# Kernel optimization log

Hardware: AMD Instinct MI355X
Metric: run time of the kernel (lower is better)

The kernel has to match this reference:

```python
import jax, jax.numpy as jnp
import numpy as np

N_LAYERS = 6
D_MODEL = 512
D_FFN = 2048
N_STATE = 64
KSIZE = 31
BATCH = 8
SEQ = 2048
IN_SIZE = 80


def _ln(x, g, b, eps=1e-5):
    m = jnp.mean(x, axis=-1, keepdims=True)
    v = jnp.mean((x - m) ** 2, axis=-1, keepdims=True)
    return (x - m) * jax.lax.rsqrt(v + eps) * g + b


def _ffn(x, g, b, w1, b1, w2, b2):
    # LayerNorm -> Linear(D->F) -> GELU -> Linear(F->D)  (PositionalwiseFeedForward)
    h = jax.nn.gelu(_ln(x, g, b) @ w1 + b1)
    return h @ w2 + b2


def _dss(x, lam_re, lam_im, c_re, c_im, d_skip, log_dt, w_out, b_out):
    # Diagonal state-space (DSS-EXP): generate length-T kernel from diagonal poles,
    # apply causal conv via FFT, skip D*u, GELU, GLU output projection.
    Bx, T, H = x.shape
    dt = jnp.exp(log_dt)
    lam = -jnp.exp(lam_re) + 1j * lam_im                        # [N] stable poles (Re<0)
    P = jnp.exp(lam[:, None] * (dt * jnp.arange(T))[None, :])   # [N, T]
    C = c_re + 1j * c_im                                        # [H, N]
    kern = jnp.einsum('hn,nt->ht', C, P).real * dt              # [H, T]
    u = x.transpose(0, 2, 1)                                    # [B, H, T]
    n = 2 * T
    y = jnp.fft.irfft(jnp.fft.rfft(u, n=n) * jnp.fft.rfft(kern, n=n), n=n)[..., :T]
    y = y + d_skip[None, :, None] * u
    y = jax.nn.gelu(y.transpose(0, 2, 1))                       # [B, T, H]
    z = y @ w_out + b_out                                       # [B, T, 2H]
    a, g = jnp.split(z, 2, axis=-1)
    return a * jax.nn.sigmoid(g)                                # GLU


def _conv_module(x, g1, b1, bw, bb, dw, db, g2, b2, lw, lb):
    # LN -> 1x1 conv to 2D + GLU -> depthwise conv (SAME, k=31) -> LN -> GELU -> Linear
    y = _ln(x, g1, b1)
    y = y @ bw.T + bb                                           # [B, T, 2D]
    a, g = jnp.split(y, 2, axis=-1)
    y = a * jax.nn.sigmoid(g)                                   # GLU over channels
    yc = y.transpose(0, 2, 1)                                   # [B, D, T]
    yc = jax.lax.conv_general_dilated(
        yc, dw[:, None, :], (1,), 'SAME',
        feature_group_count=yc.shape[1],
        dimension_numbers=('NCH', 'OIH', 'NCH'))
    yc = yc + db[None, :, None]
    y = jax.nn.gelu(_ln(yc.transpose(0, 2, 1), g2, b2))
    return y @ lw.T + lb


def _forward(src, speaker_embs, src_w, src_b,
             ffn1_ln_g, ffn1_ln_b, ffn1_w1, ffn1_b1, ffn1_w2, ffn1_b2,
             norm1_g, norm1_b,
             lam_re, lam_im, c_re, c_im, ssm_d, log_dt, dss_out_w, dss_out_b,
             conv_ln_g, conv_ln_b, bneck_w, bneck_b, dw_w, dw_b,
             conv_ln2_g, conv_ln2_b, conv_lin_w, conv_lin_b,
             ffn2_ln_g, ffn2_ln_b, ffn2_w1, ffn2_b1, ffn2_w2, ffn2_b2,
             norm2_g, norm2_b, final_g, final_b):
    x = src @ src_w + src_b                                     # custom_src_module Linear
    for i in range(N_LAYERS):
        x = x + 0.5 * _ffn(x, ffn1_ln_g[i], ffn1_ln_b[i], ffn1_w1[i], ffn1_b1[i], ffn1_w2[i], ffn1_b2[i])
        skip = x
        x = _ln(x, norm1_g[i], norm1_b[i])
        x = _dss(x, lam_re[i], lam_im[i], c_re[i], c_im[i], ssm_d[i], log_dt[i], dss_out_w[i], dss_out_b[i])
        x = x + skip
        x = x + _conv_module(x, conv_ln_g[i], conv_ln_b[i], bneck_w[i], bneck_b[i], dw_w[i], dw_b[i],
                             conv_ln2_g[i], conv_ln2_b[i], conv_lin_w[i], conv_lin_b[i])
        x = _ln(x + 0.5 * _ffn(x, ffn2_ln_g[i], ffn2_ln_b[i], ffn2_w1[i], ffn2_b1[i], ffn2_w2[i], ffn2_b2[i]),
                norm2_g[i], norm2_b[i])
    x = _ln(x, final_g, final_b, eps=1e-6)
    return x + speaker_embs


def setup_inputs() -> dict:
    key = jax.random.key(0)
    ks = iter(jax.random.split(key, 64))
    def rn(shape, s=0.02):
        return (jax.random.normal(next(ks), shape) * s).astype(jnp.float32)
    L, D, F, N, K = N_LAYERS, D_MODEL, D_FFN, N_STATE, KSIZE
    return dict(
        src=jax.random.normal(next(ks), (BATCH, SEQ, IN_SIZE), dtype=jnp.float32),
        speaker_embs=jax.random.normal(next(ks), (BATCH, 1, D), dtype=jnp.float32),
        src_w=rn((IN_SIZE, D)), src_b=jnp.zeros((D,), jnp.float32),
        ffn1_ln_g=jnp.ones((L, D), jnp.float32), ffn1_ln_b=jnp.zeros((L, D), jnp.float32),
        ffn1_w1=rn((L, D, F)), ffn1_b1=jnp.zeros((L, F), jnp.float32),
        ffn1_w2=rn((L, F, D)), ffn1_b2=jnp.zeros((L, D), jnp.float32),
        norm1_g=jnp.ones((L, D), jnp.float32), norm1_b=jnp.zeros((L, D), jnp.float32),
        lam_re=rn((L, N), 0.5), lam_im=rn((L, N), 3.0),
        c_re=rn((L, D, N), 0.1), c_im=rn((L, D, N), 0.1),
        ssm_d=rn((L, D), 1.0), log_dt=jnp.full((L,), float(np.log(0.01)), jnp.float32),
        dss_out_w=rn((L, D, 2 * D)), dss_out_b=jnp.zeros((L, 2 * D), jnp.float32),
        conv_ln_g=jnp.ones((L, D), jnp.float32), conv_ln_b=jnp.zeros((L, D), jnp.float32),
        bneck_w=rn((L, 2 * D, D)), bneck_b=jnp.zeros((L, 2 * D), jnp.float32),
        dw_w=rn((L, D, K), 0.1), dw_b=jnp.zeros((L, D), jnp.float32),
        conv_ln2_g=jnp.ones((L, D), jnp.float32), conv_ln2_b=jnp.zeros((L, D), jnp.float32),
        conv_lin_w=rn((L, D, D)), conv_lin_b=jnp.zeros((L, D), jnp.float32),
        ffn2_ln_g=jnp.ones((L, D), jnp.float32), ffn2_ln_b=jnp.zeros((L, D), jnp.float32),
        ffn2_w1=rn((L, D, F)), ffn2_b1=jnp.zeros((L, F), jnp.float32),
        ffn2_w2=rn((L, F, D)), ffn2_b2=jnp.zeros((L, D), jnp.float32),
        norm2_g=jnp.ones((L, D), jnp.float32), norm2_b=jnp.zeros((L, D), jnp.float32),
        final_g=jnp.ones((D,), jnp.float32), final_b=jnp.zeros((D,), jnp.float32),
    )


def reference(src, speaker_embs, src_w, src_b,
              ffn1_ln_g, ffn1_ln_b, ffn1_w1, ffn1_b1, ffn1_w2, ffn1_b2,
              norm1_g, norm1_b,
              lam_re, lam_im, c_re, c_im, ssm_d, log_dt, dss_out_w, dss_out_b,
              conv_ln_g, conv_ln_b, bneck_w, bneck_b, dw_w, dw_b,
              conv_ln2_g, conv_ln2_b, conv_lin_w, conv_lin_b,
              ffn2_ln_g, ffn2_ln_b, ffn2_w1, ffn2_b1, ffn2_w2, ffn2_b2,
              norm2_g, norm2_b, final_g, final_b):
    return _forward(src, speaker_embs, src_w, src_b,
                    ffn1_ln_g, ffn1_ln_b, ffn1_w1, ffn1_b1, ffn1_w2, ffn1_b2,
                    norm1_g, norm1_b,
                    lam_re, lam_im, c_re, c_im, ssm_d, log_dt, dss_out_w, dss_out_b,
                    conv_ln_g, conv_ln_b, bneck_w, bneck_b, dw_w, dw_b,
                    conv_ln2_g, conv_ln2_b, conv_lin_w, conv_lin_b,
                    ffn2_ln_g, ffn2_ln_b, ffn2_w1, ffn2_b1, ffn2_w2, ffn2_b2,
                    norm2_g, norm2_b, final_g, final_b)
```

## Files before the change

### kernel.cpp

```cpp
#include <hip/hip_runtime.h>
#include <hip/hip_bf16.h>
#include <stdint.h>


#define NL 6
#define TT 2048
#define BB 8
#define DD 512
#define FF 2048
#define ROWS (BB*TT)

typedef __attribute__((ext_vector_type(4))) float f32x4;
typedef __attribute__((ext_vector_type(8))) short s16x8;

#define DEVI __device__ __forceinline__

DEVI float bf2f(uint32_t u) { union { uint32_t i; float f; } v; v.i = u << 16; return v.f; }
DEVI uint16_t f2bf(float f) {
    union { float f; uint32_t i; } v; v.f = f;
    uint32_t x = v.i;
    return (uint16_t)((x + 0x7fffu + ((x >> 16) & 1u)) >> 16);
}
DEVI float gelu_f(float x) {
    float x3 = x * x * x;
    float a  = 0.7978845608028654f * (x + 0.044715f * x3);
    float e  = __expf(2.0f * a);
    float t  = 1.0f - 2.0f / (e + 1.0f);
    return 0.5f * x * (1.0f + t);
}
DEVI float sigm(float x) { return 1.0f / (1.0f + __expf(-x)); }

DEVI void gload16(const uint16_t* g, uint16_t* l) {
    __builtin_amdgcn_global_load_lds((const __attribute__((address_space(1))) void*)g,
                                     (__attribute__((address_space(3))) void*)l, 16, 0, 0);
}

__global__ void k_wtrans(const float* __restrict__ src, uint16_t* __restrict__ dst,
                         int K, int N) {
    __shared__ float tile[32][33];
    int l = blockIdx.z;
    const float* s = src + (size_t)l * K * N;
    uint16_t*    d = dst + (size_t)l * N * K;
    int n0 = blockIdx.x * 32, k0 = blockIdx.y * 32;
    int tx = threadIdx.x, ty = threadIdx.y;
#pragma unroll
    for (int i = 0; i < 4; i++) {
        int k = k0 + ty + i * 8;
        tile[ty + i * 8][tx] = s[(size_t)k * N + n0 + tx];
    }
    __syncthreads();
#pragma unroll
    for (int i = 0; i < 4; i++) {
        int n = n0 + ty + i * 8;
        d[(size_t)n * K + k0 + tx] = f2bf(tile[tx][ty + i * 8]);
    }
}
__global__ void k_wcvt(const float* __restrict__ src, uint16_t* __restrict__ dst, int n) {
    int i = blockIdx.x * 256 + threadIdx.x;
    if (i < n) dst[i] = f2bf(src[i]);
}
__global__ void k_dwt(const float* __restrict__ dw, float* __restrict__ dwt) {
    int i = blockIdx.x * 256 + threadIdx.x;
    int tot = NL * DD * 31;
    if (i >= tot) return;
    int l = i / (DD * 31), r = i % (DD * 31), d = r / 31, k = r % 31;
    dwt[(size_t)l * 31 * DD + k * DD + d] = dw[i];
}
__global__ void k_srcpad(const float* __restrict__ src, uint16_t* __restrict__ dst) {
    int i = blockIdx.x * 256 + threadIdx.x;
    if (i >= ROWS * 96) return;
    int r = i / 96, c = i - r * 96;
    dst[i] = (c < 80) ? f2bf(src[(size_t)r * 80 + c]) : (uint16_t)0;
}
__global__ void k_wsrcpad(const float* __restrict__ w, uint16_t* __restrict__ dst) {
    int i = blockIdx.x * 256 + threadIdx.x;
    if (i >= DD * 96) return;
    int n = i / 96, k = i - n * 96;
    dst[i] = (k < 80) ? f2bf(w[(size_t)k * DD + n]) : (uint16_t)0;
}

template <int MODE>
__global__ void k_ln(const float* __restrict__ in, void* __restrict__ outp,
                     const float* __restrict__ gam, const float* __restrict__ bet,
                     const float* __restrict__ spk, float eps) {
    int row  = blockIdx.x * 4 + (threadIdx.x >> 6);
    int lane = threadIdx.x & 63;
    const float* x = in + (size_t)row * DD;
    float4 a0 = *(const float4*)&x[lane * 4];
    float4 a1 = *(const float4*)&x[256 + lane * 4];
    float v[8] = {a0.x, a0.y, a0.z, a0.w, a1.x, a1.y, a1.z, a1.w};
    float s = 0.f, q = 0.f;
#pragma unroll
    for (int i = 0; i < 8; i++) { s += v[i]; q += v[i] * v[i]; }
#pragma unroll
    for (int m = 1; m < 64; m <<= 1) { s += __shfl_xor(s, m); q += __shfl_xor(q, m); }
    float mean = s * (1.0f / 512.0f);
    float var  = fmaxf(q * (1.0f / 512.0f) - mean * mean, 0.0f);
    float inv  = rsqrtf(var + eps);
    float4 g0 = *(const float4*)&gam[lane * 4];
    float4 g1 = *(const float4*)&gam[256 + lane * 4];
    float4 b0 = *(const float4*)&bet[lane * 4];
    float4 b1 = *(const float4*)&bet[256 + lane * 4];
    float gv[8] = {g0.x, g0.y, g0.z, g0.w, g1.x, g1.y, g1.z, g1.w};
    float bv[8] = {b0.x, b0.y, b0.z, b0.w, b1.x, b1.y, b1.z, b1.w};
    float y[8];
#pragma unroll
    for (int i = 0; i < 8; i++) y[i] = (v[i] - mean) * inv * gv[i] + bv[i];
    if (MODE == 1) {
#pragma unroll
        for (int i = 0; i < 8; i++) y[i] = gelu_f(y[i]);
    }
    if (MODE == 0 || MODE == 1) {
        uint16_t* o = (uint16_t*)outp + (size_t)row * DD;
        uint2 p0, p1;
        p0.x = (uint32_t)f2bf(y[0]) | ((uint32_t)f2bf(y[1]) << 16);
        p0.y = (uint32_t)f2bf(y[2]) | ((uint32_t)f2bf(y[3]) << 16);
        p1.x = (uint32_t)f2bf(y[4]) | ((uint32_t)f2bf(y[5]) << 16);
        p1.y = (uint32_t)f2bf(y[6]) | ((uint32_t)f2bf(y[7]) << 16);
        *(uint2*)&o[lane * 4]       = p0;
        *(uint2*)&o[256 + lane * 4] = p1;
    } else {
        float* o = (float*)outp + (size_t)row * DD;
        if (MODE == 3) {
            const float* sp = spk + (size_t)(row >> 11) * DD;
            float4 s0 = *(const float4*)&sp[lane * 4];
            float4 s1 = *(const float4*)&sp[256 + lane * 4];
            y[0] += s0.x; y[1] += s0.y; y[2] += s0.z; y[3] += s0.w;
            y[4] += s1.x; y[5] += s1.y; y[6] += s1.z; y[7] += s1.w;
        }
        *(float4*)&o[lane * 4]       = make_float4(y[0], y[1], y[2], y[3]);
        *(float4*)&o[256 + lane * 4] = make_float4(y[4], y[5], y[6], y[7]);
    }
}

template <int MODE>
__global__ __launch_bounds__(256) void k_gemm(
    const uint16_t* __restrict__ A, const uint16_t* __restrict__ Bt,
    const float* __restrict__ bias, int M, int N, int K,
    void* __restrict__ outp, float* __restrict__ X) {
    __shared__ __align__(16) uint16_t As[128 * 32];
    __shared__ __align__(16) uint16_t Bs[128 * 32];
    int tid = threadIdx.x;
    int m0 = blockIdx.x * 128, n0 = blockIdx.y * 128;
    int wave = tid >> 6, lane = tid & 63;
    int wm = (wave >> 1) * 64, wn = (wave & 1) * 64;
    int l15 = lane & 15, l16 = lane >> 4;

    const uint16_t* gA = A  + (size_t)(m0 + 32 * wave + l15) * K + l16 * 8;
    const uint16_t* gB = Bt + (size_t)(n0 + 32 * wave + l15) * K + l16 * 8;
    uint16_t* lA0 = &As[(2 * wave) * 512];
    uint16_t* lA1 = &As[(2 * wave + 1) * 512];
    uint16_t* lB0 = &Bs[(2 * wave) * 512];
    uint16_t* lB1 = &Bs[(2 * wave + 1) * 512];
    size_t rowskip = (size_t)16 * K;

    f32x4 acc[4][4];
#pragma unroll
    for (int i = 0; i < 4; i++)
#pragma unroll
        for (int j = 0; j < 4; j++) acc[i][j] = (f32x4){0.f, 0.f, 0.f, 0.f};

    for (int kt = 0; kt < K; kt += 32) {
        gload16(gA + kt, lA0);
        gload16(gA + rowskip + kt, lA1);
        gload16(gB + kt, lB0);
        gload16(gB + rowskip + kt, lB1);
        __syncthreads();
        s16x8 af[4], bfr[4];
#pragma unroll
        for (int i = 0; i < 4; i++)
            af[i] = *(const s16x8*)&As[((wave >> 1) * 4 + i) * 512 + lane * 8];
#pragma unroll
        for (int j = 0; j < 4; j++)
            bfr[j] = *(const s16x8*)&Bs[((wave & 1) * 4 + j) * 512 + lane * 8];
#pragma unroll
        for (int i = 0; i < 4; i++)
#pragma unroll
            for (int j = 0; j < 4; j++)
                acc[i][j] = __builtin_amdgcn_mfma_f32_16x16x32_bf16(af[i], bfr[j], acc[i][j], 0, 0, 0);
        __syncthreads();
    }
#pragma unroll
    for (int i = 0; i < 4; i++) {
#pragma unroll
        for (int j = 0; j < 4; j++) {
            int gcol = n0 + wn + j * 16 + l15;
            float bv = bias[gcol];
#pragma unroll
            for (int q = 0; q < 4; q++) {
                int grow = m0 + wm + i * 16 + l16 * 4 + q;
                float v = acc[i][j][q] + bv;
                if (MODE == 0) {
                    ((uint16_t*)outp)[(size_t)grow * N + gcol] = f2bf(gelu_f(v));
                } else if (MODE == 1) {
                    ((uint16_t*)outp)[(size_t)grow * N + gcol] = f2bf(v);
                } else if (MODE == 2) {
                    X[(size_t)grow * DD + gcol] += 0.5f * v;
                } else if (MODE == 3) {
                    X[(size_t)grow * DD + gcol] += v;
                } else if (MODE == 4) {
                    ((float*)outp)[(size_t)grow * DD + gcol] =
                        X[(size_t)grow * DD + gcol] + 0.5f * v;
                } else {
                    X[(size_t)grow * DD + gcol] = v;
                }
            }
        }
    }
}

__global__ void k_tpose(const uint16_t* __restrict__ in, uint16_t* __restrict__ out,
                        int R, int C) {
    __shared__ uint16_t tile[32][33];
    size_t boff = (size_t)blockIdx.z * R * C;
    int c0 = blockIdx.x * 32, r0 = blockIdx.y * 32;
    int tx = threadIdx.x, ty = threadIdx.y;
#pragma unroll
    for (int i = 0; i < 4; i++)
        tile[ty + i * 8][tx] = in[boff + (size_t)(r0 + ty + i * 8) * C + c0 + tx];
    __syncthreads();
#pragma unroll
    for (int i = 0; i < 4; i++)
        out[boff + (size_t)(c0 + ty + i * 8) * R + r0 + tx] = tile[tx][ty + i * 8];
}


__global__ __launch_bounds__(64) void k_phiprep(
        const float* __restrict__ lam_re, const float* __restrict__ lam_im,
        const float* __restrict__ log_dt, uint16_t* __restrict__ PHI,
        float* __restrict__ A64f) {
    int l = blockIdx.x, n = threadIdx.x;
    float dt = expf(log_dt[l]);
    float lr = lam_re[l * 64 + n], li = lam_im[l * 64 + n];
    float mag = expf(-expf(lr) * dt), th = li * dt;
    float Are = mag * __cosf(th), Aim = mag * __sinf(th);
    float Pre = 1.f, Pim = 0.f;
    uint16_t* ph = PHI + (size_t)l * 8192;
    for (int tau = 0; tau < 64; tau++) {
        int s = 63 - tau;
        ph[n * 64 + s]        = f2bf(Pre);
        ph[(64 + n) * 64 + s] = f2bf(Pim);
        float nr = Pre * Are - Pim * Aim;
        float ni = Pre * Aim + Pim * Are;
        Pre = nr; Pim = ni;
    }
    A64f[l * 128 + 2 * n]     = Pre;
    A64f[l * 128 + 2 * n + 1] = Pim;
}

__global__ __launch_bounds__(64) void k_gprep(
        const float* __restrict__ lam_re, const float* __restrict__ lam_im,
        const float* __restrict__ c_re, const float* __restrict__ c_im,
        const float* __restrict__ ssm_d, const float* __restrict__ log_dt,
        int l, uint16_t* __restrict__ G) {
    int h = blockIdx.x, n = threadIdx.x;
    __shared__ float klds[64];
    float dt = expf(log_dt[l]);
    float lr = lam_re[l * 64 + n], li = lam_im[l * 64 + n];
    float mag = expf(-expf(lr) * dt), th = li * dt;
    float Are = mag * __cosf(th), Aim = mag * __sinf(th);
    float Cre = c_re[(size_t)l * DD * 64 + h * 64 + n];
    float Cim = c_im[(size_t)l * DD * 64 + h * 64 + n];
    uint16_t* Gh = G + (size_t)h * 64 * 192;
    float Pre = 1.f, Pim = 0.f;
    for (int r = 0; r < 64; r++) {
        float t = Cre * Pre - Cim * Pim;
        float s = t;
        s += __shfl_xor(s, 1);  s += __shfl_xor(s, 2);  s += __shfl_xor(s, 4);
        s += __shfl_xor(s, 8);  s += __shfl_xor(s, 16); s += __shfl_xor(s, 32);
        if (n == 0) klds[r] = dt * s;
        float nr = Pre * Are - Pim * Aim;
        float ni = Pre * Aim + Pim * Are;
        float wre = dt * (Cre * nr - Cim * ni);
        float wim = dt * (Cre * ni + Cim * nr);
        Gh[r * 192 + 64 + n]  = f2bf(wre);
        Gh[r * 192 + 128 + n] = f2bf(-wim);
        Pre = nr; Pim = ni;
    }
    __syncthreads();
    float dh = ssm_d[l * DD + h];
    for (int r = 0; r < 64; r++) {
        int c = n;
        float val = (c < r) ? klds[r - c] : (c == r ? klds[0] + dh : 0.f);
        Gh[r * 192 + c] = f2bf(val);
    }
}

__global__ __launch_bounds__(256) void k_pass1(
        const uint16_t* __restrict__ u, const uint16_t* __restrict__ PHI,
        uint16_t* __restrict__ E) {
    __shared__ __align__(16) uint16_t Phs[128 * 72];
    int tid = threadIdx.x;
    for (int v = tid; v < 1024; v += 256) {
        int row = v >> 3, kb = v & 7;
        *(s16x8*)&Phs[row * 72 + kb * 8] = *(const s16x8*)&PHI[row * 64 + kb * 8];
    }
    __syncthreads();
    int wave = tid >> 6, lane = tid & 63;
    int l15 = lane & 15, l16 = lane >> 4;
    int m0 = (wave & 1) * 64;
    int colbase = blockIdx.x * 128 + (wave >> 1) * 64;
    f32x4 acc[4][4];
#pragma unroll
    for (int i = 0; i < 4; i++)
#pragma unroll
        for (int j = 0; j < 4; j++) acc[i][j] = (f32x4){0.f, 0.f, 0.f, 0.f};
#pragma unroll
    for (int kt = 0; kt < 64; kt += 32) {
        s16x8 a[4], b[4];
#pragma unroll
        for (int i = 0; i < 4; i++)
            a[i] = *(const s16x8*)&Phs[(m0 + i * 16 + l15) * 72 + kt + l16 * 8];
#pragma unroll
        for (int j = 0; j < 4; j++)
            b[j] = *(const s16x8*)(u + (size_t)(colbase + j * 16 + l15) * 64 + kt + l16 * 8);
#pragma unroll
        for (int i = 0; i < 4; i++)
#pragma unroll
            for (int j = 0; j < 4; j++)
                acc[i][j] = __builtin_amdgcn_mfma_f32_16x16x32_bf16(a[i], b[j], acc[i][j], 0, 0, 0);
    }
#pragma unroll
    for (int i = 0; i < 4; i++)
#pragma unroll
        for (int j = 0; j < 4; j++) {
            int col = colbase + j * 16 + l15;
            int r0  = m0 + i * 16 + l16 * 4;
            uint32_t p0 = (uint32_t)f2bf(acc[i][j][0]) | ((uint32_t)f2bf(acc[i][j][1]) << 16);
            uint32_t p1 = (uint32_t)f2bf(acc[i][j][2]) | ((uint32_t)f2bf(acc[i][j][3]) << 16);
            *(uint2*)&E[(size_t)col * 128 + r0] = make_uint2(p0, p1);
        }
}

__global__ void k_pass2(const uint16_t* __restrict__ E, const float* __restrict__ A64f,
                        int l, uint16_t* __restrict__ Sp) {
    int gid = blockIdx.x * 256 + threadIdx.x;
    int n = gid & 63, bh = gid >> 6;
    int b = bh >> 9, h = bh & 511;
    float2 A = *(const float2*)&A64f[l * 128 + 2 * n];
    float Sre = 0.f, Sim = 0.f;
    const uint16_t* Eb = E + (size_t)bh * 32 * 128;
    uint16_t* So = Sp + (size_t)h * 32768 + (size_t)b * 32 * 128;
    for (int i = 0; i < 32; i++) {
        So[i * 128 + n]      = f2bf(Sre);
        So[i * 128 + 64 + n] = f2bf(Sim);
        float er = bf2f((uint32_t)Eb[i * 128 + n]);
        float ei = bf2f((uint32_t)Eb[i * 128 + 64 + n]);
        float nr = A.x * Sre - A.y * Sim + er;
        float ni = A.x * Sim + A.y * Sre + ei;
        Sre = nr; Sim = ni;
    }
}

__global__ __launch_bounds__(256) void k_pass3(
        const uint16_t* __restrict__ G, const uint16_t* __restrict__ u,
        const uint16_t* __restrict__ Sp, uint16_t* __restrict__ Y) {
    __shared__ __align__(16) uint16_t Gs[64 * 200];
    int h = blockIdx.x, tid = threadIdx.x;
    for (int v = tid; v < 1536; v += 256) {
        int row = v / 24, kb = v % 24;
        *(s16x8*)&Gs[row * 200 + kb * 8] = *(const s16x8*)&G[(size_t)h * 12288 + row * 192 + kb * 8];
    }
    __syncthreads();
    int wave = tid >> 6, lane = tid & 63;
    int l15 = lane & 15, l16 = lane >> 4;
    int wn = wave * 64;
    const uint16_t* uh = u + (size_t)h * TT;
    const uint16_t* sh = Sp + (size_t)h * 32768;
    f32x4 acc[4][4];
#pragma unroll
    for (int i = 0; i < 4; i++)
#pragma unroll
        for (int j = 0; j < 4; j++) acc[i][j] = (f32x4){0.f, 0.f, 0.f, 0.f};
#pragma unroll
    for (int kt = 0; kt < 192; kt += 32) {
        s16x8 a[4], b[4];
#pragma unroll
        for (int i = 0; i < 4; i++)
            a[i] = *(const s16x8*)&Gs[(i * 16 + l15) * 200 + kt + l16 * 8];
#pragma unroll
        for (int j = 0; j < 4; j++) {
            int col = wn + j * 16 + l15;
            const uint16_t* src;
            if (kt < 64)
                src = uh + (size_t)(col >> 5) * (DD * TT) + (col & 31) * 64 + kt + l16 * 8;
            else
                src = sh + (size_t)col * 128 + (kt - 64) + l16 * 8;
            b[j] = *(const s16x8*)src;
        }
#pragma unroll
        for (int i = 0; i < 4; i++)
#pragma unroll
            for (int j = 0; j < 4; j++)
                acc[i][j] = __builtin_amdgcn_mfma_f32_16x16x32_bf16(a[i], b[j], acc[i][j], 0, 0, 0);
    }
#pragma unroll
    for (int i = 0; i < 4; i++)
#pragma unroll
        for (int j = 0; j < 4; j++) {
            int col = wn + j * 16 + l15;
            int r0  = i * 16 + l16 * 4;
            uint16_t* dst = Y + (size_t)(col >> 5) * (DD * TT) + (size_t)h * TT + (col & 31) * 64 + r0;
            uint32_t p0 = (uint32_t)f2bf(acc[i][j][0]) | ((uint32_t)f2bf(acc[i][j][1]) << 16);
            uint32_t p1 = (uint32_t)f2bf(acc[i][j][2]) | ((uint32_t)f2bf(acc[i][j][3]) << 16);
            *(uint2*)&dst[0] = make_uint2(p0, p1);
        }
}

__global__ void k_tgelu(const uint16_t* __restrict__ y, uint16_t* __restrict__ out) {
    __shared__ uint16_t tile[32][33];
    int b = blockIdx.z;
    int t0 = blockIdx.x * 32, h0 = blockIdx.y * 32;
    int tx = threadIdx.x, ty = threadIdx.y;
    const uint16_t* yb = y + (size_t)b * DD * TT;
#pragma unroll
    for (int i = 0; i < 4; i++) {
        int h = h0 + ty + i * 8;
        tile[ty + i * 8][tx] = f2bf(gelu_f(bf2f((uint32_t)yb[(size_t)h * TT + t0 + tx])));
    }
    __syncthreads();
    uint16_t* ob = out + (size_t)b * TT * DD;
#pragma unroll
    for (int i = 0; i < 4; i++) {
        int t = t0 + ty + i * 8;
        ob[(size_t)t * DD + h0 + tx] = tile[tx][ty + i * 8];
    }
}

template <int SKIP>
__global__ void k_glu(const uint16_t* __restrict__ z, float* __restrict__ X,
                      uint16_t* __restrict__ out) {
    int i = blockIdx.x * 256 + threadIdx.x;
    int r = i >> 8;
    int c = (i & 255) * 2;
    uint32_t av = *(const uint32_t*)&z[(size_t)r * 1024 + c];
    uint32_t gv = *(const uint32_t*)&z[(size_t)r * 1024 + 512 + c];
    float a0 = bf2f(av & 0xffffu), a1 = bf2f(av >> 16);
    float g0 = bf2f(gv & 0xffffu), g1 = bf2f(gv >> 16);
    float v0 = a0 * sigm(g0), v1 = a1 * sigm(g1);
    if (SKIP) {
        float2* px = (float2*)&X[(size_t)r * DD + c];
        float2 x = *px;
        x.x += v0; x.y += v1;
        *px = x;
    } else {
        uint32_t p = (uint32_t)f2bf(v0) | ((uint32_t)f2bf(v1) << 16);
        *(uint32_t*)&out[(size_t)r * DD + c] = p;
    }
}

__global__ __launch_bounds__(256) void k_dwconv(
        const uint16_t* __restrict__ in, const float* __restrict__ dwt,
        const float* __restrict__ db, float* __restrict__ out) {
    __shared__ __align__(16) uint16_t xs[34 * 512];
    int tid = threadIdx.x;
    int t0 = (blockIdx.x & 511) * 4;
    int b  = blockIdx.x >> 9;
    const uint16_t* ib = in + (size_t)b * TT * DD;
    for (int v = tid; v < 34 * 64; v += 256) {
        int row = v >> 6, seg = v & 63;
        int tj = t0 - 15 + row;
        uint4 val = make_uint4(0, 0, 0, 0);
        if (tj >= 0 && tj < TT) val = *(const uint4*)&ib[(size_t)tj * DD + seg * 8];
        *(uint4*)&xs[row * 512 + seg * 8] = val;
    }
    __syncthreads();
    int d = tid * 2;
    float a0[4], a1[4];
    float bv0 = db[d], bv1 = db[d + 1];
#pragma unroll
    for (int o = 0; o < 4; o++) { a0[o] = bv0; a1[o] = bv1; }
#pragma unroll
    for (int k = 0; k < 31; k++) {
        float2 w = *(const float2*)&dwt[k * DD + d];
#pragma unroll
        for (int o = 0; o < 4; o++) {
            uint32_t v = *(const uint32_t*)&xs[(o + k) * 512 + d];
            a0[o] = fmaf(bf2f(v & 0xffffu), w.x, a0[o]);
            a1[o] = fmaf(bf2f(v >> 16), w.y, a1[o]);
        }
    }
#pragma unroll
    for (int o = 0; o < 4; o++) {
        *(float2*)&out[((size_t)b * TT + t0 + o) * DD + d] = make_float2(a0[o], a1[o]);
    }
}

extern "C" void kernel_launch(void* const* d_in, const int* in_sizes, int n_in,
                              void* d_out, int out_size, void* d_ws, size_t ws_size,
                              hipStream_t stream) {
    const float* src        = (const float*)d_in[0];
    const float* speaker    = (const float*)d_in[1];
    const float* src_w      = (const float*)d_in[2];
    const float* src_b      = (const float*)d_in[3];
    const float* ffn1_ln_g  = (const float*)d_in[4];
    const float* ffn1_ln_b  = (const float*)d_in[5];
    const float* ffn1_w1    = (const float*)d_in[6];
    const float* ffn1_b1    = (const float*)d_in[7];
    const float* ffn1_w2    = (const float*)d_in[8];
    const float* ffn1_b2    = (const float*)d_in[9];
    const float* norm1_g    = (const float*)d_in[10];
    const float* norm1_b    = (const float*)d_in[11];
    const float* lam_re     = (const float*)d_in[12];
    const float* lam_im     = (const float*)d_in[13];
    const float* c_re       = (const float*)d_in[14];
    const float* c_im       = (const float*)d_in[15];
    const float* ssm_d      = (const float*)d_in[16];
    const float* log_dt     = (const float*)d_in[17];
    const float* dss_out_w  = (const float*)d_in[18];
    const float* dss_out_b  = (const float*)d_in[19];
    const float* conv_ln_g  = (const float*)d_in[20];
    const float* conv_ln_b  = (const float*)d_in[21];
    const float* bneck_w    = (const float*)d_in[22];
    const float* bneck_b    = (const float*)d_in[23];
    const float* dw_w       = (const float*)d_in[24];
    const float* dw_b       = (const float*)d_in[25];
    const float* conv_ln2_g = (const float*)d_in[26];
    const float* conv_ln2_b = (const float*)d_in[27];
    const float* conv_lin_w = (const float*)d_in[28];
    const float* conv_lin_b = (const float*)d_in[29];
    const float* ffn2_ln_g  = (const float*)d_in[30];
    const float* ffn2_ln_b  = (const float*)d_in[31];
    const float* ffn2_w1    = (const float*)d_in[32];
    const float* ffn2_b1    = (const float*)d_in[33];
    const float* ffn2_w2    = (const float*)d_in[34];
    const float* ffn2_b2    = (const float*)d_in[35];
    const float* norm2_g    = (const float*)d_in[36];
    const float* norm2_b    = (const float*)d_in[37];
    const float* final_g    = (const float*)d_in[38];
    const float* final_b    = (const float*)d_in[39];
    (void)in_sizes; (void)n_in; (void)out_size; (void)ws_size;

    uint8_t* ws = (uint8_t*)d_ws;
    float*    X   = (float*)   (ws + 0);
    float*    F0  = (float*)   (ws + 33554432);
    uint16_t* B1  = (uint16_t*)(ws + 67108864);
    uint16_t* B2  = (uint16_t*)(ws + 83886080);
    uint16_t* B3  = (uint16_t*)(ws + 100663296);
    uint16_t* H   = (uint16_t*)(ws + 117440512);
    uint16_t* Wf1a= (uint16_t*)(ws + 184549376);
    uint16_t* Wf1b= (uint16_t*)(ws + 197132288);
    uint16_t* Wds = (uint16_t*)(ws + 209715200);
    uint16_t* Wbn = (uint16_t*)(ws + 216006656);
    uint16_t* Wcl = (uint16_t*)(ws + 222298112);
    uint16_t* Wf2a= (uint16_t*)(ws + 225443840);
    uint16_t* Wf2b= (uint16_t*)(ws + 238026752);
    float*    DWT = (float*)   (ws + 250609664);
    uint16_t* PHI = (uint16_t*)(ws + 250990592);
    float*    A64f= (float*)   (ws + 251088896);

    uint16_t* GBUF = B1;
    uint16_t* SPK  = (uint16_t*)F0;
    uint16_t* EBUF = H;
    uint16_t* SRCB = B3;
    uint16_t* WSRC = B2;

    dim3 tb(32, 8);
    k_wtrans<<<dim3(FF/32, DD/32, NL), tb, 0, stream>>>(ffn1_w1, Wf1a, DD, FF);
    k_wtrans<<<dim3(DD/32, FF/32, NL), tb, 0, stream>>>(ffn1_w2, Wf1b, FF, DD);
    k_wtrans<<<dim3(1024/32, DD/32, NL), tb, 0, stream>>>(dss_out_w, Wds, DD, 1024);
    k_wcvt<<<(NL*1024*DD + 255)/256, 256, 0, stream>>>(bneck_w, Wbn, NL*1024*DD);
    k_wcvt<<<(NL*DD*DD + 255)/256, 256, 0, stream>>>(conv_lin_w, Wcl, NL*DD*DD);
    k_wtrans<<<dim3(FF/32, DD/32, NL), tb, 0, stream>>>(ffn2_w1, Wf2a, DD, FF);
    k_wtrans<<<dim3(DD/32, FF/32, NL), tb, 0, stream>>>(ffn2_w2, Wf2b, FF, DD);
    k_dwt<<<(NL*DD*31 + 255)/256, 256, 0, stream>>>(dw_w, DWT);
    k_phiprep<<<NL, 64, 0, stream>>>(lam_re, lam_im, log_dt, PHI, A64f);
    k_srcpad<<<(ROWS*96 + 255)/256, 256, 0, stream>>>(src, SRCB);
    k_wsrcpad<<<(DD*96 + 255)/256, 256, 0, stream>>>(src_w, WSRC);

    k_gemm<5><<<dim3(128, 4), 256, 0, stream>>>(SRCB, WSRC, src_b, ROWS, DD, 96, nullptr, X);

    for (int l = 0; l < NL; l++) {
        k_ln<0><<<4096, 256, 0, stream>>>(X, B1, ffn1_ln_g + l*DD, ffn1_ln_b + l*DD, nullptr, 1e-5f);
        k_gemm<0><<<dim3(128, 16), 256, 0, stream>>>(B1, Wf1a + (size_t)l*FF*DD, ffn1_b1 + l*FF,
                                                     ROWS, FF, DD, H, nullptr);
        k_gemm<2><<<dim3(128, 4), 256, 0, stream>>>(H, Wf1b + (size_t)l*DD*FF, ffn1_b2 + l*DD,
                                                    ROWS, DD, FF, nullptr, X);
        k_ln<0><<<4096, 256, 0, stream>>>(X, B1, norm1_g + l*DD, norm1_b + l*DD, nullptr, 1e-5f);
        k_tpose<<<dim3(DD/32, TT/32, BB), tb, 0, stream>>>(B1, B2, TT, DD);
        k_gprep<<<DD, 64, 0, stream>>>(lam_re, lam_im, c_re, c_im, ssm_d, log_dt, l, GBUF);
        k_pass1<<<1024, 256, 0, stream>>>(B2, PHI + (size_t)l*8192, EBUF);
        k_pass2<<<1024, 256, 0, stream>>>(EBUF, A64f, l, SPK);
        k_pass3<<<DD, 256, 0, stream>>>(GBUF, B2, SPK, B3);
        k_tgelu<<<dim3(TT/32, DD/32, BB), tb, 0, stream>>>(B3, B1);
        k_gemm<1><<<dim3(128, 8), 256, 0, stream>>>(B1, Wds + (size_t)l*1024*DD, dss_out_b + l*1024,
                                                    ROWS, 1024, DD, H, nullptr);
        k_glu<1><<<ROWS, 256, 0, stream>>>(H, X, nullptr);
        k_ln<0><<<4096, 256, 0, stream>>>(X, B1, conv_ln_g + l*DD, conv_ln_b + l*DD, nullptr, 1e-5f);
        k_gemm<1><<<dim3(128, 8), 256, 0, stream>>>(B1, Wbn + (size_t)l*1024*DD, bneck_b + l*1024,
                                                    ROWS, 1024, DD, H, nullptr);
        k_glu<0><<<ROWS, 256, 0, stream>>>(H, nullptr, B2);
        k_dwconv<<<BB*512, 256, 0, stream>>>(B2, DWT + (size_t)l*31*DD, dw_b + l*DD, F0);
        k_ln<1><<<4096, 256, 0, stream>>>(F0, B1, conv_ln2_g + l*DD, conv_ln2_b + l*DD, nullptr, 1e-5f);
        k_gemm<3><<<dim3(128, 4), 256, 0, stream>>>(B1, Wcl + (size_t)l*DD*DD, conv_lin_b + l*DD,
                                                    ROWS, DD, DD, nullptr, X);
        k_ln<0><<<4096, 256, 0, stream>>>(X, B1, ffn2_ln_g + l*DD, ffn2_ln_b + l*DD, nullptr, 1e-5f);
        k_gemm<0><<<dim3(128, 16), 256, 0, stream>>>(B1, Wf2a + (size_t)l*FF*DD, ffn2_b1 + l*FF,
                                                     ROWS, FF, DD, H, nullptr);
        k_gemm<4><<<dim3(128, 4), 256, 0, stream>>>(H, Wf2b + (size_t)l*DD*FF, ffn2_b2 + l*DD,
                                                    ROWS, DD, FF, F0, X);
        k_ln<2><<<4096, 256, 0, stream>>>(F0, X, norm2_g + l*DD, norm2_b + l*DD, nullptr, 1e-5f);
    }
    k_ln<3><<<4096, 256, 0, stream>>>(X, d_out, final_g, final_b, speaker, 1e-6f);
}
```

Baseline: 3.843 ms.

## Double-buffer GEMM LDS tiles and use cheaper GELU/sigmoid formulations

The GEMM main loop now ping-pongs between two LDS buffers and issues the global-to-LDS loads for the next K tile before computing on the current one. The goal is to overlap memory latency with MFMA work instead of stalling on a sync after every load. Separately, GELU is rewritten as x*sigmoid(1.5958*(x+0.0447x^3)) and both GELU and sigmoid use a hardware reciprocal in place of a division. These changes double LDS usage, which may lower occupancy, and the fast reciprocal is slightly less accurate.

```diff
diff --git a/kernel.cpp b/kernel.cpp
--- a/kernel.cpp
+++ b/kernel.cpp
@@ -22,13 +22,11 @@
     return (uint16_t)((x + 0x7fffu + ((x >> 16) & 1u)) >> 16);
 }
 DEVI float gelu_f(float x) {
-    float x3 = x * x * x;
-    float a  = 0.7978845608028654f * (x + 0.044715f * x3);
-    float e  = __expf(2.0f * a);
-    float t  = 1.0f - 2.0f / (e + 1.0f);
-    return 0.5f * x * (1.0f + t);
-}
-DEVI float sigm(float x) { return 1.0f / (1.0f + __expf(-x)); }
+    float x2 = x * x;
+    float z  = x * fmaf(x2, 0.07135481627f, 1.5957691216f);
+    return x * __builtin_amdgcn_rcpf(1.0f + __expf(-z));
+}
+DEVI float sigm(float x) { return __builtin_amdgcn_rcpf(1.0f + __expf(-x)); }
 
 DEVI void gload16(const uint16_t* g, uint16_t* l) {
     __builtin_amdgcn_global_load_lds((const __attribute__((address_space(1))) void*)g,
@@ -138,8 +136,8 @@
     const uint16_t* __restrict__ A, const uint16_t* __restrict__ Bt,
     const float* __restrict__ bias, int M, int N, int K,
     void* __restrict__ outp, float* __restrict__ X) {
-    __shared__ __align__(16) uint16_t As[128 * 32];
-    __shared__ __align__(16) uint16_t Bs[128 * 32];
+    __shared__ __align__(16) uint16_t As[2][128 * 32];
+    __shared__ __align__(16) uint16_t Bs[2][128 * 32];
     int tid = threadIdx.x;
     int m0 = blockIdx.x * 128, n0 = blockIdx.y * 128;
     int wave = tid >> 6, lane = tid & 63;
@@ -148,10 +146,6 @@
 
     const uint16_t* gA = A  + (size_t)(m0 + 32 * wave + l15) * K + l16 * 8;
     const uint16_t* gB = Bt + (size_t)(n0 + 32 * wave + l15) * K + l16 * 8;
-    uint16_t* lA0 = &As[(2 * wave) * 512];
-    uint16_t* lA1 = &As[(2 * wave + 1) * 512];
-    uint16_t* lB0 = &Bs[(2 * wave) * 512];
-    uint16_t* lB1 = &Bs[(2 * wave + 1) * 512];
     size_t rowskip = (size_t)16 * K;
 
     f32x4 acc[4][4];
@@ -160,19 +154,29 @@
 #pragma unroll
         for (int j = 0; j < 4; j++) acc[i][j] = (f32x4){0.f, 0.f, 0.f, 0.f};
 
-    for (int kt = 0; kt < K; kt += 32) {
-        gload16(gA + kt, lA0);
-        gload16(gA + rowskip + kt, lA1);
-        gload16(gB + kt, lB0);
-        gload16(gB + rowskip + kt, lB1);
-        __syncthreads();
+    gload16(gA, &As[0][(2 * wave) * 512]);
+    gload16(gA + rowskip, &As[0][(2 * wave + 1) * 512]);
+    gload16(gB, &Bs[0][(2 * wave) * 512]);
+    gload16(gB + rowskip, &Bs[0][(2 * wave + 1) * 512]);
+    __syncthreads();
+
+    int nk = K >> 5;
+    for (int it = 0; it < nk; ++it) {
+        int cur = it & 1;
+        if (it + 1 < nk) {
+            int kt = (it + 1) << 5;
+            gload16(gA + kt, &As[cur ^ 1][(2 * wave) * 512]);
+            gload16(gA + rowskip + kt, &As[cur ^ 1][(2 * wave + 1) * 512]);
+            gload16(gB + kt, &Bs[cur ^ 1][(2 * wave) * 512]);
+            gload16(gB + rowskip + kt, &Bs[cur ^ 1][(2 * wave + 1) * 512]);
+        }
         s16x8 af[4], bfr[4];
 #pragma unroll
         for (int i = 0; i < 4; i++)
-            af[i] = *(const s16x8*)&As[((wave >> 1) * 4 + i) * 512 + lane * 8];
+            af[i] = *(const s16x8*)&As[cur][((wave >> 1) * 4 + i) * 512 + lane * 8];
 #pragma unroll
         for (int j = 0; j < 4; j++)
-            bfr[j] = *(const s16x8*)&Bs[((wave & 1) * 4 + j) * 512 + lane * 8];
+            bfr[j] = *(const s16x8*)&Bs[cur][((wave & 1) * 4 + j) * 512 + lane * 8];
 #pragma unroll
         for (int i = 0; i < 4; i++)
 #pragma unroll
```

Result: faster. 3.675 ms (-4.4%).
